# Kernel tuning notes

Measured on AMD Instinct MI355X. Metric: run time of the kernel, lower is better.

The kernel has to match this reference:

```python
import jax, jax.numpy as jnp
import numpy as np

N, E, F_IN, H, C = 100000, 1250000, 512, 64, 40
K = 2


def _lin_w(key, fan_out, fan_in):
    bound = 1.0 / np.sqrt(fan_in)
    return jax.random.uniform(key, (fan_out, fan_in), jnp.float32, -bound, bound)


def setup_inputs() -> dict:
    key = jax.random.key(0)
    ks = jax.random.split(key, 14)
    x = jax.random.normal(ks[0], (N, F_IN), dtype=jnp.float32)
    edge_index = jax.random.randint(ks[1], (2, E), 0, N, dtype=jnp.int64)
    inp = {
        "x": x,
        "edge_index": edge_index,
        "W_in": _lin_w(ks[2], H, F_IN),
        "b_in": jnp.zeros((H,), jnp.float32),
        "W1_0": _lin_w(ks[3], H, H),
        "W2_0": _lin_w(ks[4], H, H),
        "Wf_0": _lin_w(ks[5], H, H),
        "W1_1": _lin_w(ks[6], H, H),
        "W2_1": _lin_w(ks[7], H, H),
        "Wf_1": _lin_w(ks[8], H, H),
        "W_out": _lin_w(ks[9], C, H),
        "b_out": jnp.zeros((C,), jnp.float32),
    }
    return inp


def _step_conv(Q, row, col, W1, W2, Wf, n):
    # StepConv.forward with step == 0 (the only valid branch in the source)
    h3 = Q @ W1.T              # [N, H]
    h4 = Q @ W2.T              # [N, H]
    hloop = jax.nn.relu(Q @ Wf.T)
    # edge gate: s = sigmoid(-<h3[row], h4[col]>)  per edge
    s = jax.nn.sigmoid(-jnp.sum(h3[row] * h4[col], axis=1))  # [E]
    # propagate (source_to_target): scatter messages from row into col
    agg3 = jax.ops.segment_sum(s[:, None] * h3[row], col, num_segments=n)
    agg4 = jax.ops.segment_sum((1.0 - s)[:, None] * h4[row], col, num_segments=n)
    return hloop + agg3 - agg4


def reference(x, edge_index, W_in, b_in, W1_0, W2_0, Wf_0, W1_1, W2_1, Wf_1, W_out, b_out):
    n = x.shape[0]
    row, col = edge_index[0], edge_index[1]
    Q = x @ W_in.T + b_in
    for (W1, W2, Wf) in ((W1_0, W2_0, Wf_0), (W1_1, W2_1, Wf_1)):
        hq3 = _step_conv(Q, row, col, W1, W2, Wf, n)
        # F.normalize(p=2, dim=1), eps=1e-12
        Q = hq3 / jnp.maximum(jnp.linalg.norm(hq3, axis=1, keepdims=True), 1e-12)
    logits = Q @ W_out.T + b_out
    return jax.nn.log_softmax(logits, axis=1)
```

## Files before the change

### kernel.cpp

```cpp
#include <hip/hip_runtime.h>
#include <hip/hip_bf16.h>
#include <math.h>

#define H 64
#define FIN 512
#define COUT 40

typedef __attribute__((ext_vector_type(8))) short bf16x8;
typedef __attribute__((ext_vector_type(4))) float f32x4;

__device__ __forceinline__ unsigned short f2bf(float f) {
    union { float f; unsigned u; } v; v.f = f;
    unsigned r = v.u + 0x7FFF + ((v.u >> 16) & 1);
    return (unsigned short)(r >> 16);
}
__device__ __forceinline__ float bflo(unsigned u) { return __uint_as_float(u << 16); }
__device__ __forceinline__ float bfhi(unsigned u) { return __uint_as_float(u & 0xffff0000u); }

__global__ void k_pack(const float* __restrict__ W_in,
                       const float* __restrict__ W1_0, const float* __restrict__ W2_0,
                       const float* __restrict__ Wf_0,
                       const float* __restrict__ W1_1, const float* __restrict__ W2_1,
                       const float* __restrict__ Wf_1,
                       const float* __restrict__ W_out,
                       uint4* __restrict__ Bp, uint4* __restrict__ Bc0,
                       uint4* __restrict__ Bc1, uint4* __restrict__ Bo) {
    int t = blockIdx.x * blockDim.x + threadIdx.x;
    const float* src;
    uint4* dst;
    if (t < 4096) {
        int kb = t >> 6, n = t & 63;
        src = &W_in[n * FIN + kb * 8];
        dst = &Bp[t];
    } else if (t < 4096 + 1536) {
        int u = t - 4096;
        int j = u >> 9, kb = (u >> 6) & 7, n = u & 63;
        const float* W = (j == 0) ? W1_0 : (j == 1) ? W2_0 : Wf_0;
        src = &W[n * H + kb * 8];
        dst = &Bc0[u];
    } else if (t < 4096 + 3072) {
        int u = t - 4096 - 1536;
        int j = u >> 9, kb = (u >> 6) & 7, n = u & 63;
        const float* W = (j == 0) ? W1_1 : (j == 1) ? W2_1 : Wf_1;
        src = &W[n * H + kb * 8];
        dst = &Bc1[u];
    } else if (t < 4096 + 3072 + 512) {
        int u = t - 4096 - 3072;
        int kb = u >> 6, col = u & 63;
        if (col >= COUT) { Bo[u] = make_uint4(0u, 0u, 0u, 0u); return; }
        src = &W_out[col * H + kb * 8];
        dst = &Bo[u];
    } else return;
    float4 a0 = *(const float4*)&src[0];
    float4 a1 = *(const float4*)&src[4];
    uint4 u;
    u.x = ((unsigned)f2bf(a0.y) << 16) | f2bf(a0.x);
    u.y = ((unsigned)f2bf(a0.w) << 16) | f2bf(a0.z);
    u.z = ((unsigned)f2bf(a1.y) << 16) | f2bf(a1.x);
    u.w = ((unsigned)f2bf(a1.w) << 16) | f2bf(a1.z);
    *dst = u;
}

__global__ void k_zero(int* __restrict__ p, int n) {
    int i = blockIdx.x * blockDim.x + threadIdx.x;
    if (i < n) p[i] = 0;
}

__global__ void k_hist(const int* __restrict__ ei, int* __restrict__ deg, int nE) {
    int e = blockIdx.x * blockDim.x + threadIdx.x;
    if (e < nE) atomicAdd(&deg[ei[nE + e]], 1);
}

__global__ __launch_bounds__(256) void k_scan1(const int* __restrict__ deg, int* __restrict__ epos,
                                               int* __restrict__ blocksum, int n) {
    __shared__ int tmp[256];
    int t = threadIdx.x;
    int base = blockIdx.x * 1024 + t * 4;
    int v[4]; int s = 0;
#pragma unroll
    for (int i = 0; i < 4; ++i) { v[i] = (base + i < n) ? deg[base + i] : 0; s += v[i]; }
    tmp[t] = s;
    __syncthreads();
    int incl = s;
    for (int off = 1; off < 256; off <<= 1) {
        int y = (t >= off) ? tmp[t - off] : 0;
        __syncthreads();
        incl += y;
        tmp[t] = incl;
        __syncthreads();
    }
    if (t == 255) blocksum[blockIdx.x] = incl;
    int run = incl - s;
#pragma unroll
    for (int i = 0; i < 4; ++i) { if (base + i < n) epos[base + i] = run; run += v[i]; }
}

__global__ __launch_bounds__(256) void k_scan2(const int* __restrict__ blocksum,
                                               int* __restrict__ blockoff, int nb) {
    __shared__ int tmp[256];
    int t = threadIdx.x;
    int s = (t < nb) ? blocksum[t] : 0;
    tmp[t] = s;
    __syncthreads();
    int incl = s;
    for (int off = 1; off < 256; off <<= 1) {
        int y = (t >= off) ? tmp[t - off] : 0;
        __syncthreads();
        incl += y;
        tmp[t] = incl;
        __syncthreads();
    }
    if (t < nb) blockoff[t] = incl - s;
}

__global__ __launch_bounds__(256) void k_scan3(int* __restrict__ epos, const int* __restrict__ blockoff,
                                               int* __restrict__ cursor, int n, int nE) {
    int b = blockIdx.x;
    int off = blockoff[b];
    int base = b * 1024 + threadIdx.x * 4;
#pragma unroll
    for (int i = 0; i < 4; ++i) {
        if (base + i < n) {
            int p = epos[base + i] + off;
            epos[base + i] = p;
            cursor[base + i] = p;
        }
    }
    if (b == 0 && threadIdx.x == 0) epos[n] = nE;
}

__global__ void k_scatter(const int* __restrict__ ei, int* __restrict__ cursor,
                          int* __restrict__ srcidx, int nE) {
    int e = blockIdx.x * blockDim.x + threadIdx.x;
    if (e < nE) {
        int c = ei[nE + e];
        int p = atomicAdd(&cursor[c], 1);
        srcidx[p] = ei[e];
    }
}

__global__ __launch_bounds__(256) void k_in_gemm(
    const float* __restrict__ x, const uint4* __restrict__ Bp,
    const float* __restrict__ bias, unsigned short* __restrict__ qbf, int n) {
    __shared__ uint4 As4[256];
    __shared__ uint4 Bs4[256];
    int tid = threadIdx.x;
    int base = blockIdx.x * 64;
    int lane = tid & 63, w = tid >> 6;

    int srow = tid >> 2;
    int sg = tid & 3;
    int sgs = sg ^ ((srow >> 1) & 3);
    bool rowok = (base + srow) < n;
    const float* xsrc = &x[(size_t)(base + srow) * FIN + sg * 8];

    int arow = 16 * w + (lane & 15);
    int ag = (lane >> 4) ^ ((arow >> 1) & 3);
    int aidx = arow * 4 + ag;
    int kg = lane >> 4;

    f32x4 acc[4];
#pragma unroll
    for (int i = 0; i < 4; ++i) acc[i] = (f32x4){0.f, 0.f, 0.f, 0.f};

    for (int kk = 0; kk < FIN; kk += 32) {
        float4 a0 = make_float4(0.f, 0.f, 0.f, 0.f), a1 = a0;
        if (rowok) {
            a0 = *(const float4*)&xsrc[kk];
            a1 = *(const float4*)&xsrc[kk + 4];
        }
        uint4 bstage = Bp[((kk >> 3) + (tid >> 6)) * 64 + (tid & 63)];
        __syncthreads();
        {
            uint4 u;
            u.x = ((unsigned)f2bf(a0.y) << 16) | f2bf(a0.x);
            u.y = ((unsigned)f2bf(a0.w) << 16) | f2bf(a0.z);
            u.z = ((unsigned)f2bf(a1.y) << 16) | f2bf(a1.x);
            u.w = ((unsigned)f2bf(a1.w) << 16) | f2bf(a1.z);
            As4[srow * 4 + sgs] = u;
            Bs4[tid] = bstage;
        }
        __syncthreads();
        bf16x8 af = *(const bf16x8*)&As4[aidx];
#pragma unroll
        for (int nt = 0; nt < 4; ++nt) {
            bf16x8 bfr = *(const bf16x8*)&Bs4[kg * 64 + nt * 16 + (lane & 15)];
            acc[nt] = __builtin_amdgcn_mfma_f32_16x16x32_bf16(af, bfr, acc[nt], 0, 0, 0);
        }
    }
    int col0 = lane & 15, rowg = lane >> 4;
#pragma unroll
    for (int nt = 0; nt < 4; ++nt) {
        float bv = bias[nt * 16 + col0];
#pragma unroll
        for (int reg = 0; reg < 4; ++reg) {
            int r = base + 16 * w + rowg * 4 + reg;
            if (r < n) qbf[(size_t)r * H + nt * 16 + col0] = f2bf(acc[nt][reg] + bv);
        }
    }
}

__global__ __launch_bounds__(256) void k_layer_gemm(
    const uint4* __restrict__ Qbf, const uint4* __restrict__ Bc,
    unsigned* __restrict__ P, unsigned short* __restrict__ hl, int n) {
    __shared__ uint4 Qs[512];
    int tid = threadIdx.x;
    int base = blockIdx.x * 64;
    int lane = tid & 63, w = tid >> 6;
    {
        int r = tid >> 2, g0 = (tid & 3) * 2;
        uint4 u0 = make_uint4(0u, 0u, 0u, 0u), u1 = u0;
        if (base + r < n) {
            u0 = Qbf[(size_t)(base + r) * 8 + g0];
            u1 = Qbf[(size_t)(base + r) * 8 + g0 + 1];
        }
        Qs[r * 8 + (g0 ^ (r & 7))] = u0;
        Qs[r * 8 + ((g0 + 1) ^ (r & 7))] = u1;
    }
    __syncthreads();

    int arow = w * 16 + (lane & 15);
    f32x4 acc[12];
#pragma unroll
    for (int i = 0; i < 12; ++i) acc[i] = (f32x4){0.f, 0.f, 0.f, 0.f};

#pragma unroll
    for (int ks = 0; ks < 2; ++ks) {
        int g = ks * 4 + (lane >> 4);
        bf16x8 af = *(const bf16x8*)&Qs[arow * 8 + (g ^ (arow & 7))];
#pragma unroll
        for (int j = 0; j < 3; ++j) {
#pragma unroll
            for (int nt = 0; nt < 4; ++nt) {
                bf16x8 bfr = *(const bf16x8*)&Bc[(j * 8 + g) * 64 + nt * 16 + (lane & 15)];
                acc[j * 4 + nt] = __builtin_amdgcn_mfma_f32_16x16x32_bf16(af, bfr, acc[j * 4 + nt], 0, 0, 0);
            }
        }
    }
    int col0 = lane & 15, rowg = lane >> 4;
#pragma unroll
    for (int nt = 0; nt < 4; ++nt) {
#pragma unroll
        for (int reg = 0; reg < 4; ++reg) {
            int r = base + w * 16 + rowg * 4 + reg;
            if (r < n) {
                int col = nt * 16 + col0;
                unsigned pv = ((unsigned)f2bf(acc[4 + nt][reg]) << 16) | f2bf(acc[nt][reg]);
                P[(size_t)r * H + col] = pv;
                hl[(size_t)r * H + col] = f2bf(fmaxf(acc[8 + nt][reg], 0.f));
            }
        }
    }
}

__global__ __launch_bounds__(256) void k_agg(
    const int* __restrict__ rowptr, const int* __restrict__ srcidx,
    const unsigned* __restrict__ P, const unsigned* __restrict__ hl32,
    unsigned* __restrict__ Qbf32, int n) {
    int tid = threadIdx.x;
    int lane = tid & 63;
    int w = tid >> 6;
    int c = blockIdx.x * 4 + w;
    if (c >= n) return;
    int q = lane >> 4;
    int j = lane & 15;
    const uint4* P4 = (const uint4*)P;

    uint4 pc = P4[(size_t)c * 16 + j];
    float4 h4c = make_float4(bfhi(pc.x), bfhi(pc.y), bfhi(pc.z), bfhi(pc.w));
    float4 acc = make_float4(0.f, 0.f, 0.f, 0.f);

    int k0 = rowptr[c], k1 = rowptr[c + 1];
    if (k0 < k1) {
        const uint4 Z = make_uint4(0u, 0u, 0u, 0u);
        int last = k1 - 1;
        int e0 = k0 + q;
        int sA = srcidx[min(e0, last)];
        bool vA = e0 < k1;
        int sB = srcidx[min(e0 + 4, last)];
        bool vB = (e0 + 4) < k1;
        uint4 pA = P4[(size_t)sA * 16 + j];
        if (!vA) pA = Z;

        for (int kb = k0; kb < k1; kb += 4) {
            int e2 = kb + 8 + q;
            int sC = srcidx[min(e2, last)];
            bool vC = e2 < k1;
            uint4 pB = P4[(size_t)sB * 16 + j];
            if (!vB) pB = Z;
            float4 h3r = make_float4(bflo(pA.x), bflo(pA.y), bflo(pA.z), bflo(pA.w));
            float4 h4r = make_float4(bfhi(pA.x), bfhi(pA.y), bfhi(pA.z), bfhi(pA.w));
            float d = h3r.x * h4c.x + h3r.y * h4c.y + h3r.z * h4c.z + h3r.w * h4c.w;
            d += __shfl_xor(d, 1, 64);
            d += __shfl_xor(d, 2, 64);
            d += __shfl_xor(d, 4, 64);
            d += __shfl_xor(d, 8, 64);
            float s = 1.0f / (1.0f + __expf(d));
            float t = 1.0f - s;
            acc.x += s * h3r.x - t * h4r.x;
            acc.y += s * h3r.y - t * h4r.y;
            acc.z += s * h3r.z - t * h4r.z;
            acc.w += s * h3r.w - t * h4r.w;
            pA = pB; sB = sC; vB = vC;
        }
    }
    acc.x += __shfl_xor(acc.x, 16, 64);
    acc.y += __shfl_xor(acc.y, 16, 64);
    acc.z += __shfl_xor(acc.z, 16, 64);
    acc.w += __shfl_xor(acc.w, 16, 64);
    acc.x += __shfl_xor(acc.x, 32, 64);
    acc.y += __shfl_xor(acc.y, 32, 64);
    acc.z += __shfl_xor(acc.z, 32, 64);
    acc.w += __shfl_xor(acc.w, 32, 64);

    uint2 hv = *(const uint2*)&hl32[(size_t)c * 32 + j * 2];
    acc.x += bflo(hv.x); acc.y += bfhi(hv.x);
    acc.z += bflo(hv.y); acc.w += bfhi(hv.y);

    float ss = acc.x * acc.x + acc.y * acc.y + acc.z * acc.z + acc.w * acc.w;
    ss += __shfl_xor(ss, 1, 64);
    ss += __shfl_xor(ss, 2, 64);
    ss += __shfl_xor(ss, 4, 64);
    ss += __shfl_xor(ss, 8, 64);
    float inv = 1.0f / fmaxf(sqrtf(ss), 1e-12f);

    if (lane < 16) {
        uint2 o;
        o.x = ((unsigned)f2bf(acc.y * inv) << 16) | f2bf(acc.x * inv);
        o.y = ((unsigned)f2bf(acc.w * inv) << 16) | f2bf(acc.z * inv);
        *(uint2*)&Qbf32[(size_t)c * 32 + j * 2] = o;
    }
}

__global__ __launch_bounds__(256) void k_head(
    const uint4* __restrict__ Qbf, const uint4* __restrict__ Bo,
    const float* __restrict__ b_out, float* __restrict__ out, int n) {
    __shared__ uint4 Qs[512];
    int tid = threadIdx.x;
    int base = blockIdx.x * 64;
    int lane = tid & 63, w = tid >> 6;
    {
        int r = tid >> 2, g0 = (tid & 3) * 2;
        uint4 u0 = make_uint4(0u, 0u, 0u, 0u), u1 = u0;
        if (base + r < n) {
            u0 = Qbf[(size_t)(base + r) * 8 + g0];
            u1 = Qbf[(size_t)(base + r) * 8 + g0 + 1];
        }
        Qs[r * 8 + (g0 ^ (r & 7))] = u0;
        Qs[r * 8 + ((g0 + 1) ^ (r & 7))] = u1;
    }
    __syncthreads();

    int arow = w * 16 + (lane & 15);
    f32x4 acc[3];
#pragma unroll
    for (int i = 0; i < 3; ++i) acc[i] = (f32x4){0.f, 0.f, 0.f, 0.f};
#pragma unroll
    for (int ks = 0; ks < 2; ++ks) {
        int g = ks * 4 + (lane >> 4);
        bf16x8 af = *(const bf16x8*)&Qs[arow * 8 + (g ^ (arow & 7))];
#pragma unroll
        for (int nt = 0; nt < 3; ++nt) {
            bf16x8 bfr = *(const bf16x8*)&Bo[g * 64 + nt * 16 + (lane & 15)];
            acc[nt] = __builtin_amdgcn_mfma_f32_16x16x32_bf16(af, bfr, acc[nt], 0, 0, 0);
        }
    }
    int col = lane & 15, rowg = lane >> 4;
    float bv0 = b_out[col];
    float bv1 = b_out[16 + col];
    float bv2 = (col < 8) ? b_out[32 + col] : 0.f;
#pragma unroll
    for (int reg = 0; reg < 4; ++reg) {
        int r = base + w * 16 + rowg * 4 + reg;
        float v0 = acc[0][reg] + bv0;
        float v1 = acc[1][reg] + bv1;
        float v2 = (col < 8) ? (acc[2][reg] + bv2) : -3.0e38f;
        float m = fmaxf(fmaxf(v0, v1), v2);
        m = fmaxf(m, __shfl_xor(m, 1, 64));
        m = fmaxf(m, __shfl_xor(m, 2, 64));
        m = fmaxf(m, __shfl_xor(m, 4, 64));
        m = fmaxf(m, __shfl_xor(m, 8, 64));
        float ex = __expf(v0 - m) + __expf(v1 - m) + ((col < 8) ? __expf(v2 - m) : 0.f);
        ex += __shfl_xor(ex, 1, 64);
        ex += __shfl_xor(ex, 2, 64);
        ex += __shfl_xor(ex, 4, 64);
        ex += __shfl_xor(ex, 8, 64);
        float lse = m + logf(ex);
        if (r < n) {
            out[(size_t)r * COUT + col] = v0 - lse;
            out[(size_t)r * COUT + 16 + col] = v1 - lse;
            if (col < 8) out[(size_t)r * COUT + 32 + col] = v2 - lse;
        }
    }
}

extern "C" void kernel_launch(void* const* d_in, const int* in_sizes, int n_in,
                              void* d_out, int out_size, void* d_ws, size_t ws_size,
                              hipStream_t stream) {
    const float* x     = (const float*)d_in[0];
    const int*   ei    = (const int*)d_in[1];
    const float* W_in  = (const float*)d_in[2];
    const float* b_in  = (const float*)d_in[3];
    const float* W1_0  = (const float*)d_in[4];
    const float* W2_0  = (const float*)d_in[5];
    const float* Wf_0  = (const float*)d_in[6];
    const float* W1_1  = (const float*)d_in[7];
    const float* W2_1  = (const float*)d_in[8];
    const float* Wf_1  = (const float*)d_in[9];
    const float* W_out = (const float*)d_in[10];
    const float* b_out = (const float*)d_in[11];
    float* out = (float*)d_out;

    int N = in_sizes[0] / FIN;
    int E = in_sizes[1] / 2;

    uint4* Bp    = (uint4*)d_ws;
    uint4* Bc0   = Bp + 4096;
    uint4* Bc1   = Bc0 + 1536;
    uint4* Bo    = Bc1 + 1536;
    unsigned* Qbf32 = (unsigned*)(Bo + 512);
    unsigned* P  = Qbf32 + (size_t)N * 32;
    unsigned* hl32 = P + (size_t)N * H;
    int* rowptr  = (int*)(hl32 + (size_t)N * 32);
    int* deg     = rowptr + (N + 2);
    int* cursor  = deg + N;
    int* srcidx  = cursor + N;
    int* blocksum = srcidx + E;
    int* blockoff = blocksum + 256;

    k_pack<<<30, 256, 0, stream>>>(W_in, W1_0, W2_0, Wf_0, W1_1, W2_1, Wf_1, W_out,
                                   Bp, Bc0, Bc1, Bo);

    int nb = (N + 1023) / 1024;
    k_zero<<<(N + 255) / 256, 256, 0, stream>>>(deg, N);
    k_hist<<<(E + 255) / 256, 256, 0, stream>>>(ei, deg, E);
    k_scan1<<<nb, 256, 0, stream>>>(deg, rowptr, blocksum, N);
    k_scan2<<<1, 256, 0, stream>>>(blocksum, blockoff, nb);
    k_scan3<<<nb, 256, 0, stream>>>(rowptr, blockoff, cursor, N, E);
    k_scatter<<<(E + 255) / 256, 256, 0, stream>>>(ei, cursor, srcidx, E);

    int gm = (N + 63) / 64;
    k_in_gemm<<<gm, 256, 0, stream>>>(x, Bp, b_in, (unsigned short*)Qbf32, N);

    int ga = (N + 3) / 4;
    k_layer_gemm<<<gm, 256, 0, stream>>>((const uint4*)Qbf32, Bc0, P, (unsigned short*)hl32, N);
    k_agg<<<ga, 256, 0, stream>>>(rowptr, srcidx, P, hl32, Qbf32, N);
    k_layer_gemm<<<gm, 256, 0, stream>>>((const uint4*)Qbf32, Bc1, P, (unsigned short*)hl32, N);
    k_agg<<<ga, 256, 0, stream>>>(rowptr, srcidx, P, hl32, Qbf32, N);
    k_head<<<gm, 256, 0, stream>>>((const uint4*)Qbf32, Bo, b_out, out, N);
}
```

Before: 352.6 us.

## Pad CSR segments to multiples of four with dummy zero row, drop bounds checks

Each node's edge list is padded to a multiple of four, and the padding slots point to an extra zero row appended to P. Source indices are pre-multiplied by 16, so the aggregation loop drops its min/valid predication and index scaling. Float-to-bf16 packing is also switched to the library's paired conversion intrinsic. The cost is extra padded edges to process, a new fill kernel, and a larger workspace layout.

```diff
diff --git a/kernel.cpp b/kernel.cpp
--- a/kernel.cpp
+++ b/kernel.cpp
@@ -13,6 +13,11 @@
     union { float f; unsigned u; } v; v.f = f;
     unsigned r = v.u + 0x7FFF + ((v.u >> 16) & 1);
     return (unsigned short)(r >> 16);
+}
+__device__ __forceinline__ unsigned pk2(float lo, float hi) {
+    __hip_bfloat162 h = __float22bfloat162_rn(make_float2(lo, hi));
+    union { __hip_bfloat162 h; unsigned u; } v; v.h = h;
+    return v.u;
 }
 __device__ __forceinline__ float bflo(unsigned u) { return __uint_as_float(u << 16); }
 __device__ __forceinline__ float bfhi(unsigned u) { return __uint_as_float(u & 0xffff0000u); }
@@ -54,10 +59,10 @@
     float4 a0 = *(const float4*)&src[0];
     float4 a1 = *(const float4*)&src[4];
     uint4 u;
-    u.x = ((unsigned)f2bf(a0.y) << 16) | f2bf(a0.x);
-    u.y = ((unsigned)f2bf(a0.w) << 16) | f2bf(a0.z);
-    u.z = ((unsigned)f2bf(a1.y) << 16) | f2bf(a1.x);
-    u.w = ((unsigned)f2bf(a1.w) << 16) | f2bf(a1.z);
+    u.x = pk2(a0.x, a0.y);
+    u.y = pk2(a0.z, a0.w);
+    u.z = pk2(a1.x, a1.y);
+    u.w = pk2(a1.z, a1.w);
     *dst = u;
 }
 
@@ -78,7 +83,10 @@
     int base = blockIdx.x * 1024 + t * 4;
     int v[4]; int s = 0;
 #pragma unroll
-    for (int i = 0; i < 4; ++i) { v[i] = (base + i < n) ? deg[base + i] : 0; s += v[i]; }
+    for (int i = 0; i < 4; ++i) {
+        v[i] = (base + i < n) ? ((deg[base + i] + 3) & ~3) : 0;
+        s += v[i];
+    }
     tmp[t] = s;
     __syncthreads();
     int incl = s;
@@ -96,7 +104,8 @@
 }
 
 __global__ __launch_bounds__(256) void k_scan2(const int* __restrict__ blocksum,
-                                               int* __restrict__ blockoff, int nb) {
+                                               int* __restrict__ blockoff, int nb,
+                                               int* __restrict__ total_out) {
     __shared__ int tmp[256];
     int t = threadIdx.x;
     int s = (t < nb) ? blocksum[t] : 0;
@@ -111,10 +120,11 @@
         __syncthreads();
     }
     if (t < nb) blockoff[t] = incl - s;
+    if (t == nb - 1) *total_out = incl;
 }
 
 __global__ __launch_bounds__(256) void k_scan3(int* __restrict__ epos, const int* __restrict__ blockoff,
-                                               int* __restrict__ cursor, int n, int nE) {
+                                               int* __restrict__ cursor, int n) {
     int b = blockIdx.x;
     int off = blockoff[b];
     int base = b * 1024 + threadIdx.x * 4;
@@ -126,7 +136,22 @@
             cursor[base + i] = p;
         }
     }
-    if (b == 0 && threadIdx.x == 0) epos[n] = nE;
+}
+
+__global__ void k_fill_dummy(const int* __restrict__ rowptr, const int* __restrict__ deg,
+                             int* __restrict__ srcidx, unsigned* __restrict__ P, int n) {
+    int i = blockIdx.x * blockDim.x + threadIdx.x;
+    int dummy = n * 16;
+    if (i < n) {
+        int s = rowptr[i] + deg[i];
+        int e = rowptr[i + 1];
+        for (int k = s; k < e; ++k) srcidx[k] = dummy;
+    }
+    if (i == 0) {
+        int t = rowptr[n];
+        for (int k = 0; k < 8; ++k) srcidx[t + k] = dummy;
+    }
+    if (i < 64) P[(size_t)n * H + i] = 0u;
 }
 
 __global__ void k_scatter(const int* __restrict__ ei, int* __restrict__ cursor,
@@ -135,7 +160,7 @@
     if (e < nE) {
         int c = ei[nE + e];
         int p = atomicAdd(&cursor[c], 1);
-        srcidx[p] = ei[e];
+        srcidx[p] = ei[e] * 16;
     }
 }
 
@@ -173,10 +198,10 @@
         __syncthreads();
         {
             uint4 u;
-            u.x = ((unsigned)f2bf(a0.y) << 16) | f2bf(a0.x);
-            u.y = ((unsigned)f2bf(a0.w) << 16) | f2bf(a0.z);
-            u.z = ((unsigned)f2bf(a1.y) << 16) | f2bf(a1.x);
-            u.w = ((unsigned)f2bf(a1.w) << 16) | f2bf(a1.z);
+            u.x = pk2(a0.x, a0.y);
+            u.y = pk2(a0.z, a0.w);
+            u.z = pk2(a1.x, a1.y);
+            u.w = pk2(a1.z, a1.w);
             As4[srow * 4 + sgs] = u;
             Bs4[tid] = bstage;
         }
@@ -245,8 +270,7 @@
             int r = base + w * 16 + rowg * 4 + reg;
             if (r < n) {
                 int col = nt * 16 + col0;
-                unsigned pv = ((unsigned)f2bf(acc[4 + nt][reg]) << 16) | f2bf(acc[nt][reg]);
-                P[(size_t)r * H + col] = pv;
+                P[(size_t)r * H + col] = pk2(acc[nt][reg], acc[4 + nt][reg]);
                 hl[(size_t)r * H + col] = f2bf(fmaxf(acc[8 + nt][reg], 0.f));
             }
         }
@@ -272,22 +296,13 @@
 
     int k0 = rowptr[c], k1 = rowptr[c + 1];
     if (k0 < k1) {
-        const uint4 Z = make_uint4(0u, 0u, 0u, 0u);
-        int last = k1 - 1;
-        int e0 = k0 + q;
-        int sA = srcidx[min(e0, last)];
-        bool vA = e0 < k1;
-        int sB = srcidx[min(e0 + 4, last)];
-        bool vB = (e0 + 4) < k1;
-        uint4 pA = P4[(size_t)sA * 16 + j];
-        if (!vA) pA = Z;
+        int sA = srcidx[k0 + q];
+        int sB = srcidx[k0 + 4 + q];
+        uint4 pA = P4[(size_t)(sA + j)];
 
         for (int kb = k0; kb < k1; kb += 4) {
-            int e2 = kb + 8 + q;
-            int sC = srcidx[min(e2, last)];
-            bool vC = e2 < k1;
-            uint4 pB = P4[(size_t)sB * 16 + j];
-            if (!vB) pB = Z;
+            int sC = srcidx[kb + 8 + q];
+            uint4 pB = P4[(size_t)(sB + j)];
             float4 h3r = make_float4(bflo(pA.x), bflo(pA.y), bflo(pA.z), bflo(pA.w));
             float4 h4r = make_float4(bfhi(pA.x), bfhi(pA.y), bfhi(pA.z), bfhi(pA.w));
             float d = h3r.x * h4c.x + h3r.y * h4c.y + h3r.z * h4c.z + h3r.w * h4c.w;
@@ -301,7 +316,7 @@
             acc.y += s * h3r.y - t * h4r.y;
             acc.z += s * h3r.z - t * h4r.z;
             acc.w += s * h3r.w - t * h4r.w;
-            pA = pB; sB = sC; vB = vC;
+            pA = pB; sB = sC;
         }
     }
     acc.x += __shfl_xor(acc.x, 16, 64);
@@ -326,8 +341,8 @@
 
     if (lane < 16) {
         uint2 o;
-        o.x = ((unsigned)f2bf(acc.y * inv) << 16) | f2bf(acc.x * inv);
-        o.y = ((unsigned)f2bf(acc.w * inv) << 16) | f2bf(acc.z * inv);
+        o.x = pk2(acc.x * inv, acc.y * inv);
+        o.y = pk2(acc.z * inv, acc.w * inv);
         *(uint2*)&Qbf32[(size_t)c * 32 + j * 2] = o;
     }
 }
@@ -420,12 +435,12 @@
     uint4* Bo    = Bc1 + 1536;
     unsigned* Qbf32 = (unsigned*)(Bo + 512);
     unsigned* P  = Qbf32 + (size_t)N * 32;
-    unsigned* hl32 = P + (size_t)N * H;
+    unsigned* hl32 = P + (size_t)(N + 1) * H;
     int* rowptr  = (int*)(hl32 + (size_t)N * 32);
     int* deg     = rowptr + (N + 2);
     int* cursor  = deg + N;
     int* srcidx  = cursor + N;
-    int* blocksum = srcidx + E;
+    int* blocksum = srcidx + E + 3 * N + 16;
     int* blockoff = blocksum + 256;
 
     k_pack<<<30, 256, 0, stream>>>(W_in, W1_0, W2_0, Wf_0, W1_1, W2_1, Wf_1, W_out,
@@ -435,8 +450,9 @@
     k_zero<<<(N + 255) / 256, 256, 0, stream>>>(deg, N);
     k_hist<<<(E + 255) / 256, 256, 0, stream>>>(ei, deg, E);
     k_scan1<<<nb, 256, 0, stream>>>(deg, rowptr, blocksum, N);
-    k_scan2<<<1, 256, 0, stream>>>(blocksum, blockoff, nb);
-    k_scan3<<<nb, 256, 0, stream>>>(rowptr, blockoff, cursor, N, E);
+    k_scan2<<<1, 256, 0, stream>>>(blocksum, blockoff, nb, &rowptr[N]);
+    k_scan3<<<nb, 256, 0, stream>>>(rowptr, blockoff, cursor, N);
+    k_fill_dummy<<<(N + 255) / 256, 256, 0, stream>>>(rowptr, deg, srcidx, P, N);
     k_scatter<<<(E + 255) / 256, 256, 0, stream>>>(ei, cursor, srcidx, E);
 
     int gm = (N + 63) / 64;
```

Result: slower. 374.0 us (+6.1%).

## Recompute source-node h3/h4 per edge via MFMA instead of gathering precomputed P

Applied to the files above, without the earlier changes.

The layer GEMM now writes only h4 and the relu self-loop term. The aggregation kernel gathers the 128-byte bf16 Q rows of source nodes and recomputes h3 and h4 per edge with MFMA, using the W1/W2 weights staged in shared memory. This halves the bytes gathered per edge (previously 256-byte packed h3/h4 rows) at the cost of extra matrix math on every edge, plus a persistent grid-stride launch and ping-pong Q buffers. Nodes with low degree waste MFMA lanes, since each batch of 16 edges is padded.

```diff
diff --git a/kernel.cpp b/kernel.cpp
--- a/kernel.cpp
+++ b/kernel.cpp
@@ -14,8 +14,9 @@
     unsigned r = v.u + 0x7FFF + ((v.u >> 16) & 1);
     return (unsigned short)(r >> 16);
 }
-__device__ __forceinline__ float bflo(unsigned u) { return __uint_as_float(u << 16); }
-__device__ __forceinline__ float bfhi(unsigned u) { return __uint_as_float(u & 0xffff0000u); }
+__device__ __forceinline__ float bf2f(unsigned short u) {
+    return __uint_as_float((unsigned)u << 16);
+}
 
 __global__ void k_pack(const float* __restrict__ W_in,
                        const float* __restrict__ W1_0, const float* __restrict__ W2_0,
@@ -202,7 +203,7 @@
 
 __global__ __launch_bounds__(256) void k_layer_gemm(
     const uint4* __restrict__ Qbf, const uint4* __restrict__ Bc,
-    unsigned* __restrict__ P, unsigned short* __restrict__ hl, int n) {
+    unsigned short* __restrict__ h4bf, unsigned short* __restrict__ hl, int n) {
     __shared__ uint4 Qs[512];
     int tid = threadIdx.x;
     int base = blockIdx.x * 64;
@@ -220,20 +221,21 @@
     __syncthreads();
 
     int arow = w * 16 + (lane & 15);
-    f32x4 acc[12];
-#pragma unroll
-    for (int i = 0; i < 12; ++i) acc[i] = (f32x4){0.f, 0.f, 0.f, 0.f};
+    f32x4 acc[8];
+#pragma unroll
+    for (int i = 0; i < 8; ++i) acc[i] = (f32x4){0.f, 0.f, 0.f, 0.f};
 
 #pragma unroll
     for (int ks = 0; ks < 2; ++ks) {
         int g = ks * 4 + (lane >> 4);
         bf16x8 af = *(const bf16x8*)&Qs[arow * 8 + (g ^ (arow & 7))];
 #pragma unroll
-        for (int j = 0; j < 3; ++j) {
+        for (int m = 0; m < 2; ++m) {
+            int j = m + 1;
 #pragma unroll
             for (int nt = 0; nt < 4; ++nt) {
                 bf16x8 bfr = *(const bf16x8*)&Bc[(j * 8 + g) * 64 + nt * 16 + (lane & 15)];
-                acc[j * 4 + nt] = __builtin_amdgcn_mfma_f32_16x16x32_bf16(af, bfr, acc[j * 4 + nt], 0, 0, 0);
+                acc[m * 4 + nt] = __builtin_amdgcn_mfma_f32_16x16x32_bf16(af, bfr, acc[m * 4 + nt], 0, 0, 0);
             }
         }
     }
@@ -245,9 +247,8 @@
             int r = base + w * 16 + rowg * 4 + reg;
             if (r < n) {
                 int col = nt * 16 + col0;
-                unsigned pv = ((unsigned)f2bf(acc[4 + nt][reg]) << 16) | f2bf(acc[nt][reg]);
-                P[(size_t)r * H + col] = pv;
-                hl[(size_t)r * H + col] = f2bf(fmaxf(acc[8 + nt][reg], 0.f));
+                h4bf[(size_t)r * H + col] = f2bf(acc[nt][reg]);
+                hl[(size_t)r * H + col] = f2bf(fmaxf(acc[4 + nt][reg], 0.f));
             }
         }
     }
@@ -255,80 +256,87 @@
 
 __global__ __launch_bounds__(256) void k_agg(
     const int* __restrict__ rowptr, const int* __restrict__ srcidx,
-    const unsigned* __restrict__ P, const unsigned* __restrict__ hl32,
-    unsigned* __restrict__ Qbf32, int n) {
+    const uint4* __restrict__ Qin4, const unsigned short* __restrict__ h4bf,
+    const unsigned short* __restrict__ hl, unsigned short* __restrict__ Qout,
+    const uint4* __restrict__ Bc, int n) {
+    __shared__ uint4 Ws[1024];
     int tid = threadIdx.x;
-    int lane = tid & 63;
-    int w = tid >> 6;
-    int c = blockIdx.x * 4 + w;
-    if (c >= n) return;
-    int q = lane >> 4;
-    int j = lane & 15;
-    const uint4* P4 = (const uint4*)P;
-
-    uint4 pc = P4[(size_t)c * 16 + j];
-    float4 h4c = make_float4(bfhi(pc.x), bfhi(pc.y), bfhi(pc.z), bfhi(pc.w));
-    float4 acc = make_float4(0.f, 0.f, 0.f, 0.f);
-
-    int k0 = rowptr[c], k1 = rowptr[c + 1];
-    if (k0 < k1) {
-        const uint4 Z = make_uint4(0u, 0u, 0u, 0u);
+    for (int i = tid; i < 1024; i += 256) Ws[i] = Bc[i];
+    __syncthreads();
+
+    int lane = tid & 63, w = tid >> 6;
+    int l15 = lane & 15, g = lane >> 4;
+
+    for (int c = blockIdx.x * 4 + w; c < n; c += gridDim.x * 4) {
+        float h4c[4], accQ[4];
+#pragma unroll
+        for (int nt = 0; nt < 4; ++nt) {
+            h4c[nt] = bf2f(h4bf[(size_t)c * H + nt * 16 + l15]);
+            accQ[nt] = 0.f;
+        }
+        int k0 = rowptr[c], k1 = rowptr[c + 1];
         int last = k1 - 1;
-        int e0 = k0 + q;
-        int sA = srcidx[min(e0, last)];
-        bool vA = e0 < k1;
-        int sB = srcidx[min(e0 + 4, last)];
-        bool vB = (e0 + 4) < k1;
-        uint4 pA = P4[(size_t)sA * 16 + j];
-        if (!vA) pA = Z;
-
-        for (int kb = k0; kb < k1; kb += 4) {
-            int e2 = kb + 8 + q;
-            int sC = srcidx[min(e2, last)];
-            bool vC = e2 < k1;
-            uint4 pB = P4[(size_t)sB * 16 + j];
-            if (!vB) pB = Z;
-            float4 h3r = make_float4(bflo(pA.x), bflo(pA.y), bflo(pA.z), bflo(pA.w));
-            float4 h4r = make_float4(bfhi(pA.x), bfhi(pA.y), bfhi(pA.z), bfhi(pA.w));
-            float d = h3r.x * h4c.x + h3r.y * h4c.y + h3r.z * h4c.z + h3r.w * h4c.w;
-            d += __shfl_xor(d, 1, 64);
-            d += __shfl_xor(d, 2, 64);
-            d += __shfl_xor(d, 4, 64);
-            d += __shfl_xor(d, 8, 64);
-            float s = 1.0f / (1.0f + __expf(d));
-            float t = 1.0f - s;
-            acc.x += s * h3r.x - t * h4r.x;
-            acc.y += s * h3r.y - t * h4r.y;
-            acc.z += s * h3r.z - t * h4r.z;
-            acc.w += s * h3r.w - t * h4r.w;
-            pA = pB; sB = sC; vB = vC;
-        }
-    }
-    acc.x += __shfl_xor(acc.x, 16, 64);
-    acc.y += __shfl_xor(acc.y, 16, 64);
-    acc.z += __shfl_xor(acc.z, 16, 64);
-    acc.w += __shfl_xor(acc.w, 16, 64);
-    acc.x += __shfl_xor(acc.x, 32, 64);
-    acc.y += __shfl_xor(acc.y, 32, 64);
-    acc.z += __shfl_xor(acc.z, 32, 64);
-    acc.w += __shfl_xor(acc.w, 32, 64);
-
-    uint2 hv = *(const uint2*)&hl32[(size_t)c * 32 + j * 2];
-    acc.x += bflo(hv.x); acc.y += bfhi(hv.x);
-    acc.z += bflo(hv.y); acc.w += bfhi(hv.y);
-
-    float ss = acc.x * acc.x + acc.y * acc.y + acc.z * acc.z + acc.w * acc.w;
-    ss += __shfl_xor(ss, 1, 64);
-    ss += __shfl_xor(ss, 2, 64);
-    ss += __shfl_xor(ss, 4, 64);
-    ss += __shfl_xor(ss, 8, 64);
-    float inv = 1.0f / fmaxf(sqrtf(ss), 1e-12f);
-
-    if (lane < 16) {
-        uint2 o;
-        o.x = ((unsigned)f2bf(acc.y * inv) << 16) | f2bf(acc.x * inv);
-        o.y = ((unsigned)f2bf(acc.w * inv) << 16) | f2bf(acc.z * inv);
-        *(uint2*)&Qbf32[(size_t)c * 32 + j * 2] = o;
+
+        for (int kb = k0; kb < k1; kb += 16) {
+            int e = kb + l15;
+            int idx = srcidx[min(e, last)];
+            uint4 a0 = Qin4[(size_t)idx * 8 + g];
+            uint4 a1 = Qin4[(size_t)idx * 8 + 4 + g];
+
+            f32x4 acc3[4], acc4[4];
+#pragma unroll
+            for (int nt = 0; nt < 4; ++nt) {
+                acc3[nt] = (f32x4){0.f, 0.f, 0.f, 0.f};
+                acc4[nt] = (f32x4){0.f, 0.f, 0.f, 0.f};
+            }
+#pragma unroll
+            for (int ks = 0; ks < 2; ++ks) {
+                bf16x8 af = ks ? *(const bf16x8*)&a1 : *(const bf16x8*)&a0;
+                int kbase = (ks * 4 + g) * 64;
+#pragma unroll
+                for (int nt = 0; nt < 4; ++nt) {
+                    bf16x8 b1 = *(const bf16x8*)&Ws[kbase + nt * 16 + l15];
+                    bf16x8 b2 = *(const bf16x8*)&Ws[512 + kbase + nt * 16 + l15];
+                    acc3[nt] = __builtin_amdgcn_mfma_f32_16x16x32_bf16(af, b1, acc3[nt], 0, 0, 0);
+                    acc4[nt] = __builtin_amdgcn_mfma_f32_16x16x32_bf16(af, b2, acc4[nt], 0, 0, 0);
+                }
+            }
+            int bs = g * 4;
+#pragma unroll
+            for (int r = 0; r < 4; ++r) {
+                float d = acc3[0][r] * h4c[0] + acc3[1][r] * h4c[1]
+                        + acc3[2][r] * h4c[2] + acc3[3][r] * h4c[3];
+                d += __shfl_xor(d, 1, 64);
+                d += __shfl_xor(d, 2, 64);
+                d += __shfl_xor(d, 4, 64);
+                d += __shfl_xor(d, 8, 64);
+                float s = 1.0f / (1.0f + __expf(d));
+                bool valid = (kb + bs + r) < k1;
+                float sv = valid ? s : 0.f;
+                float tv = valid ? (1.0f - s) : 0.f;
+#pragma unroll
+                for (int nt = 0; nt < 4; ++nt)
+                    accQ[nt] += sv * acc3[nt][r] - tv * acc4[nt][r];
+            }
+        }
+#pragma unroll
+        for (int nt = 0; nt < 4; ++nt) {
+            accQ[nt] += __shfl_xor(accQ[nt], 16, 64);
+            accQ[nt] += __shfl_xor(accQ[nt], 32, 64);
+            accQ[nt] += bf2f(hl[(size_t)c * H + nt * 16 + l15]);
+        }
+        float ss = accQ[0] * accQ[0] + accQ[1] * accQ[1]
+                 + accQ[2] * accQ[2] + accQ[3] * accQ[3];
+        ss += __shfl_xor(ss, 1, 64);
+        ss += __shfl_xor(ss, 2, 64);
+        ss += __shfl_xor(ss, 4, 64);
+        ss += __shfl_xor(ss, 8, 64);
+        float inv = 1.0f / fmaxf(sqrtf(ss), 1e-12f);
+        if (lane < 16) {
+#pragma unroll
+            for (int nt = 0; nt < 4; ++nt)
+                Qout[(size_t)c * H + nt * 16 + lane] = f2bf(accQ[nt] * inv);
+        }
     }
 }
 
@@ -418,10 +426,11 @@
     uint4* Bc0   = Bp + 4096;
     uint4* Bc1   = Bc0 + 1536;
     uint4* Bo    = Bc1 + 1536;
-    unsigned* Qbf32 = (unsigned*)(Bo + 512);
-    unsigned* P  = Qbf32 + (size_t)N * 32;
-    unsigned* hl32 = P + (size_t)N * H;
-    int* rowptr  = (int*)(hl32 + (size_t)N * 32);
+    unsigned* Q0 = (unsigned*)(Bo + 512);
+    unsigned* Q1 = Q0 + (size_t)N * 32;
+    unsigned* h4 = Q1 + (size_t)N * 32;
+    unsigned* hl = h4 + (size_t)N * 32;
+    int* rowptr  = (int*)(hl + (size_t)N * 32);
     int* deg     = rowptr + (N + 2);
     int* cursor  = deg + N;
     int* srcidx  = cursor + N;
@@ -440,12 +449,17 @@
     k_scatter<<<(E + 255) / 256, 256, 0, stream>>>(ei, cursor, srcidx, E);
 
     int gm = (N + 63) / 64;
-    k_in_gemm<<<gm, 256, 0, stream>>>(x, Bp, b_in, (unsigned short*)Qbf32, N);
-
-    int ga = (N + 3) / 4;
-    k_layer_gemm<<<gm, 256, 0, stream>>>((const uint4*)Qbf32, Bc0, P, (unsigned short*)hl32, N);
-    k_agg<<<ga, 256, 0, stream>>>(rowptr, srcidx, P, hl32, Qbf32, N);
-    k_layer_gemm<<<gm, 256, 0, stream>>>((const uint4*)Qbf32, Bc1, P, (unsigned short*)hl32, N);
-    k_agg<<<ga, 256, 0, stream>>>(rowptr, srcidx, P, hl32, Qbf32, N);
-    k_head<<<gm, 256, 0, stream>>>((const uint4*)Qbf32, Bo, b_out, out, N);
-}
+    k_in_gemm<<<gm, 256, 0, stream>>>(x, Bp, b_in, (unsigned short*)Q0, N);
+
+    k_layer_gemm<<<gm, 256, 0, stream>>>((const uint4*)Q0, Bc0,
+                                         (unsigned short*)h4, (unsigned short*)hl, N);
+    k_agg<<<1024, 256, 0, stream>>>(rowptr, srcidx, (const uint4*)Q0,
+                                    (const unsigned short*)h4, (const unsigned short*)hl,
+                                    (unsigned short*)Q1, Bc0, N);
+    k_layer_gemm<<<gm, 256, 0, stream>>>((const uint4*)Q1, Bc1,
+                                         (unsigned short*)h4, (unsigned short*)hl, N);
+    k_agg<<<1024, 256, 0, stream>>>(rowptr, srcidx, (const uint4*)Q1,
+                                    (const unsigned short*)h4, (const unsigned short*)hl,
+                                    (unsigned short*)Q0, Bc1, N);
+    k_head<<<gm, 256, 0, stream>>>((const uint4*)Q0, Bo, b_out, out, N);
+}
```

Result: slower. 509.7 us (+44.5%).
